# Optimization experiments

Hardware: AMD Instinct MI355X
Metric: run time of the kernel (lower is better)

## Reference

```python
import jax, jax.numpy as jnp
import numpy as np

N_NODES = 50000
N_EDGES = 800000
D_IN, D_HID, D_ENC = 256, 128, 64


def setup_inputs() -> dict:
    key = jax.random.key(0)
    ks = jax.random.split(key, 8)
    x = jax.random.normal(ks[0], (N_NODES, D_IN), dtype=jnp.float32)
    edge_index = jax.random.randint(ks[1], (2, N_EDGES), 0, N_NODES, dtype=jnp.int64)
    # GCNConv params: lin weight (no bias) + separate bias, stored as [in, out]
    W1 = jax.random.normal(ks[2], (D_IN, D_HID), dtype=jnp.float32) * (1.0 / np.sqrt(D_IN))
    b1 = jnp.zeros((D_HID,), dtype=jnp.float32)
    W2 = jax.random.normal(ks[3], (D_HID, D_ENC), dtype=jnp.float32) * (1.0 / np.sqrt(D_HID))
    b2 = jnp.zeros((D_ENC,), dtype=jnp.float32)
    Wfc = jax.random.normal(ks[4], (D_ENC, 1), dtype=jnp.float32) * (1.0 / np.sqrt(D_ENC))
    bfc = jnp.zeros((1,), dtype=jnp.float32)
    return {"x": x, "edge_index": edge_index, "W1": W1, "b1": b1,
            "W2": W2, "b2": b2, "Wfc": Wfc, "bfc": bfc}


def gcn_conv(x, W, b, row, col, norm, n_nodes):
    """PyG GCNConv (normalize=True): D^-1/2 (A+I) D^-1/2 X W + b."""
    h = x @ W                                   # [N, out]
    msg = h[row] * norm[:, None]                # [E+N, out] gather + scale
    out = jax.ops.segment_sum(msg, col, num_segments=n_nodes)  # scatter-add
    return out + b


def gcn_norm(edge_index, n_nodes, dtype):
    loop = jnp.arange(n_nodes, dtype=edge_index.dtype)
    row = jnp.concatenate([edge_index[0], loop])  # sources
    col = jnp.concatenate([edge_index[1], loop])  # targets
    deg = jax.ops.segment_sum(jnp.ones_like(col, dtype=dtype), col,
                              num_segments=n_nodes)
    dinv = jnp.where(deg > 0, jax.lax.rsqrt(jnp.maximum(deg, 1e-12)), 0.0)
    norm = dinv[row] * dinv[col]
    return row, col, norm


def reference(x, edge_index, W1, b1, W2, b2, Wfc, bfc):
    n = x.shape[0]
    row, col, norm = gcn_norm(edge_index, n, x.dtype)
    h = gcn_conv(x, W1, b1, row, col, norm, n)
    h = jax.nn.relu(h)
    # dropout p=0 / eval mode: identity
    h = gcn_conv(h, W2, b2, row, col, norm, n)
    out = jax.nn.sigmoid(h @ Wfc + bfc)          # [N, 1]
    return out
```

## Files before the change

### kernel.cpp

```cpp
#include <hip/hip_runtime.h>
#include <cmath>

#define N_NODES 50000
#define N_EDGES 800000
#define D_IN 256
#define D_HID 128
#define D_ENC 64
#define NBUK 128
#define BSH 9
#define BMSK 511
#define BCAP 16384
#define PB_EPT 8

typedef short short8 __attribute__((ext_vector_type(8)));
typedef float floatx4 __attribute__((ext_vector_type(4)));
typedef float floatx8 __attribute__((ext_vector_type(8)));
typedef unsigned short ushort8v __attribute__((ext_vector_type(8)));

static __device__ __forceinline__ unsigned short f2bf(float f) {
    unsigned int u = __float_as_uint(f);
    unsigned int r = (u + 0x7FFFu + ((u >> 16) & 1u)) >> 16;
    return (unsigned short)r;
}
static __device__ __forceinline__ float bf2f(unsigned short u) {
    return __uint_as_float(((unsigned int)u) << 16);
}
static __device__ __forceinline__ floatx8 bf2f8(ushort8v u) {
    floatx8 f;
#pragma unroll
    for (int j = 0; j < 8; ++j) f[j] = bf2f(u[j]);
    return f;
}

static __device__ __forceinline__ void wswz(const float* __restrict__ W,
                                            unsigned short* __restrict__ Wsw,
                                            int t, int K, int N) {
    int KS = K / 32;
    int lane = t & 63;
    int ks   = (t >> 6) % KS;
    int ct   = (t >> 6) / KS;
    int m = lane & 15, quad = lane >> 4;
    int kbase = ks * 32 + quad * 8;
    int col   = ct * 16 + m;
#pragma unroll
    for (int j = 0; j < 8; ++j)
        Wsw[t * 8 + j] = f2bf(W[(size_t)(kbase + j) * N + col]);
}

__global__ void part_k(const int* __restrict__ rows, const int* __restrict__ cols,
                       int* __restrict__ bcur, unsigned int* __restrict__ brecs,
                       const float* __restrict__ W1, const float* __restrict__ W2,
                       unsigned short* __restrict__ Wsw1, unsigned short* __restrict__ Wsw2) {
    __shared__ int h[NBUK], base[NBUK];
    int t = blockIdx.x * blockDim.x + threadIdx.x;
    if (t < 4096) wswz(W1, Wsw1, t, D_IN, D_HID);
    else if (t < 5120) wswz(W2, Wsw2, t - 4096, D_HID, D_ENC);

    int e0 = blockIdx.x * (256 * PB_EPT);
    if (threadIdx.x < NBUK) h[threadIdx.x] = 0;
    __syncthreads();
    int src[PB_EPT], dst[PB_EPT];
#pragma unroll
    for (int j = 0; j < PB_EPT; ++j) {
        int e = e0 + j * 256 + threadIdx.x;
        if (e < N_EDGES) {
            src[j] = rows[e]; dst[j] = cols[e];
            atomicAdd(&h[dst[j] >> BSH], 1);
        } else dst[j] = -1;
    }
    __syncthreads();
    if (threadIdx.x < NBUK) {
        int c = h[threadIdx.x];
        base[threadIdx.x] = threadIdx.x * BCAP + (c ? atomicAdd(&bcur[threadIdx.x], c) : 0);
        h[threadIdx.x] = 0;
    }
    __syncthreads();
#pragma unroll
    for (int j = 0; j < PB_EPT; ++j) {
        if (dst[j] >= 0) {
            int b = dst[j] >> BSH;
            int r = base[b] + atomicAdd(&h[b], 1);
            if (r < (b + 1) * BCAP)
                brecs[r] = ((unsigned int)src[j] << BSH) | (unsigned int)(dst[j] & BMSK);
        }
    }
}

__global__ __launch_bounds__(512) void bucket_csr_k(const unsigned int* __restrict__ brecs,
                                                    const int* __restrict__ bcur,
                                                    int* __restrict__ rowptr,
                                                    int* __restrict__ rowcnt,
                                                    int* __restrict__ srcs,
                                                    float* __restrict__ dinv) {
    __shared__ int s[512];
    __shared__ int cur[512];
    int b = blockIdx.x;
    int cb = bcur[b]; if (cb > BCAP) cb = BCAP;
    int ebeg = b * BCAP, eend = ebeg + cb;
    int tid = threadIdx.x;
    s[tid] = 0;
    __syncthreads();
    for (int e = ebeg + tid; e < eend; e += 512)
        atomicAdd(&s[brecs[e] & BMSK], 1);
    __syncthreads();
    int v = s[tid];
    for (int off = 1; off < 512; off <<= 1) {
        int t = (tid >= off) ? s[tid - off] : 0;
        __syncthreads();
        s[tid] += t;
        __syncthreads();
    }
    int excl = s[tid] - v;
    cur[tid] = excl;
    int node = (b << BSH) + tid;
    if (node < N_NODES) {
        rowptr[node] = ebeg + excl;
        rowcnt[node] = v;
        dinv[node] = rsqrtf((float)(v + 1));
    }
    __syncthreads();
    for (int e = ebeg + tid; e < eend; e += 512) {
        unsigned int rec = brecs[e];
        int p = atomicAdd(&cur[rec & BMSK], 1);
        srcs[ebeg + p] = (int)(rec >> BSH);
    }
}

template<int K, int N, bool IN_BF16>
__global__ __launch_bounds__(256) void gemm_mfma_k(const void* __restrict__ Xv,
                                                   const unsigned short* __restrict__ Wsw,
                                                   const float* __restrict__ dinv,
                                                   unsigned short* __restrict__ H, int n) {
    constexpr int KS = K / 32, CT = N / 16, KP = K + 8;
    __shared__ unsigned short As[64 * KP];
    int row0 = blockIdx.x * 64;
    if (IN_BF16) {
        const ushort8v* X8 = (const ushort8v*)Xv;
        constexpr int NF8 = 64 * (K / 8);
        for (int idx = threadIdx.x; idx < NF8; idx += 256) {
            int r = idx / (K / 8), c8 = idx % (K / 8);
            int gr = row0 + r;
            ushort8v v = (gr < n) ? X8[(size_t)gr * (K / 8) + c8] : (ushort8v)0;
            *(ushort8v*)&As[r * KP + c8 * 8] = v;
        }
    } else {
        const float4* X4 = (const float4*)Xv;
        constexpr int NF4 = 64 * (K / 4);
        for (int idx = threadIdx.x; idx < NF4; idx += 256) {
            int r = idx / (K / 4), c4 = idx % (K / 4);
            int gr = row0 + r;
            float4 v = (gr < n) ? X4[(size_t)gr * (K / 4) + c4] : float4{0, 0, 0, 0};
            ushort4 p;
            p.x = f2bf(v.x); p.y = f2bf(v.y); p.z = f2bf(v.z); p.w = f2bf(v.w);
            *(ushort4*)&As[r * KP + c4 * 4] = p;
        }
    }
    __syncthreads();

    int w    = threadIdx.x >> 6;
    int lane = threadIdx.x & 63;
    int m    = lane & 15;
    int quad = lane >> 4;

    floatx4 acc[CT];
#pragma unroll
    for (int ct = 0; ct < CT; ++ct)
#pragma unroll
        for (int i = 0; i < 4; ++i) acc[ct][i] = 0.0f;

#pragma unroll
    for (int ks = 0; ks < KS; ++ks) {
        short8 af = *(const short8*)&As[(w * 16 + m) * KP + ks * 32 + quad * 8];
#pragma unroll
        for (int ct = 0; ct < CT; ++ct) {
            short8 bf = *(const short8*)&Wsw[(size_t)((ct * KS + ks) * 64 + lane) * 8];
            acc[ct] = __builtin_amdgcn_mfma_f32_16x16x32_bf16(af, bf, acc[ct], 0, 0, 0);
        }
    }

    int rbase = row0 + w * 16 + quad * 4;
    float dv[4];
#pragma unroll
    for (int reg = 0; reg < 4; ++reg) {
        int r = rbase + reg;
        dv[reg] = (r < n) ? dinv[r] : 0.0f;
    }
#pragma unroll
    for (int ct = 0; ct < CT; ++ct)
#pragma unroll
        for (int reg = 0; reg < 4; ++reg) {
            int r = rbase + reg;
            if (r < n) H[(size_t)r * N + ct * 16 + m] = f2bf(acc[ct][reg] * dv[reg]);
        }
}

__global__ __launch_bounds__(256) void g1g2_k(const ushort8v* __restrict__ hs,
                                              const int* __restrict__ rowptr,
                                              const int* __restrict__ rowcnt,
                                              const int* __restrict__ srcs,
                                              const float* __restrict__ dinv,
                                              const float4* __restrict__ b1_4,
                                              const unsigned short* __restrict__ Wsw2,
                                              unsigned short* __restrict__ h2) {
    constexpr int KP = D_HID + 8;
    __shared__ unsigned short As[16 * KP];
    int nodeb = blockIdx.x * 16;
    int ln = threadIdx.x >> 4;
    int d8 = threadIdx.x & 15;
    int node = nodeb + ln;
    int beg = rowptr[node];
    int end = beg + rowcnt[node];
    floatx8 a0 = {0,0,0,0,0,0,0,0}, a1 = a0, a2 = a0, a3 = a0;
    int i = beg;
    for (; i + 4 <= end; i += 4) {
        int s0 = srcs[i], s1 = srcs[i + 1], s2 = srcs[i + 2], s3 = srcs[i + 3];
        a0 += bf2f8(hs[(size_t)s0 * 16 + d8]);
        a1 += bf2f8(hs[(size_t)s1 * 16 + d8]);
        a2 += bf2f8(hs[(size_t)s2 * 16 + d8]);
        a3 += bf2f8(hs[(size_t)s3 * 16 + d8]);
    }
    for (; i < end; ++i)
        a0 += bf2f8(hs[(size_t)srcs[i] * 16 + d8]);
    floatx8 acc = a0 + a1 + a2 + a3 + bf2f8(hs[(size_t)node * 16 + d8]);
    float di = dinv[node];
    float4 bA = b1_4[d8 * 2], bB = b1_4[d8 * 2 + 1];
    ushort8v r;
    r[0] = f2bf(fmaxf(di * acc[0] + bA.x, 0.0f));
    r[1] = f2bf(fmaxf(di * acc[1] + bA.y, 0.0f));
    r[2] = f2bf(fmaxf(di * acc[2] + bA.z, 0.0f));
    r[3] = f2bf(fmaxf(di * acc[3] + bA.w, 0.0f));
    r[4] = f2bf(fmaxf(di * acc[4] + bB.x, 0.0f));
    r[5] = f2bf(fmaxf(di * acc[5] + bB.y, 0.0f));
    r[6] = f2bf(fmaxf(di * acc[6] + bB.z, 0.0f));
    r[7] = f2bf(fmaxf(di * acc[7] + bB.w, 0.0f));
    *(ushort8v*)&As[ln * KP + d8 * 8] = r;
    __syncthreads();

    constexpr int KS = D_HID / 32;
    int w    = threadIdx.x >> 6;
    int lane = threadIdx.x & 63;
    int m = lane & 15, quad = lane >> 4;
    floatx4 acc2 = {0, 0, 0, 0};
#pragma unroll
    for (int ks = 0; ks < KS; ++ks) {
        short8 af = *(const short8*)&As[m * KP + ks * 32 + quad * 8];
        short8 bf = *(const short8*)&Wsw2[(size_t)((w * KS + ks) * 64 + lane) * 8];
        acc2 = __builtin_amdgcn_mfma_f32_16x16x32_bf16(af, bf, acc2, 0, 0, 0);
    }
#pragma unroll
    for (int reg = 0; reg < 4; ++reg) {
        int nn = nodeb + quad * 4 + reg;
        h2[(size_t)nn * D_ENC + w * 16 + m] = f2bf(acc2[reg] * dinv[nn]);
    }
}

__global__ void gather2_k(const ushort8v* __restrict__ hs, const int* __restrict__ rowptr,
                          const int* __restrict__ rowcnt, const int* __restrict__ srcs,
                          const float* __restrict__ dinv,
                          const float4* __restrict__ b4, const float4* __restrict__ Wfc4,
                          const float* __restrict__ bfc, float* __restrict__ out) {
    int node = blockIdx.x * 32 + (threadIdx.x >> 3);
    int d8   = threadIdx.x & 7;
    if (node >= N_NODES) return;
    int beg = rowptr[node];
    int end = beg + rowcnt[node];
    floatx8 a0 = {0,0,0,0,0,0,0,0}, a1 = a0, a2 = a0, a3 = a0;
    int i = beg;
    for (; i + 4 <= end; i += 4) {
        int s0 = srcs[i], s1 = srcs[i + 1], s2 = srcs[i + 2], s3 = srcs[i + 3];
        a0 += bf2f8(hs[(size_t)s0 * 8 + d8]);
        a1 += bf2f8(hs[(size_t)s1 * 8 + d8]);
        a2 += bf2f8(hs[(size_t)s2 * 8 + d8]);
        a3 += bf2f8(hs[(size_t)s3 * 8 + d8]);
    }
    for (; i < end; ++i)
        a0 += bf2f8(hs[(size_t)srcs[i] * 8 + d8]);
    floatx8 acc = a0 + a1 + a2 + a3 + bf2f8(hs[(size_t)node * 8 + d8]);
    float di = dinv[node];
    float4 bA = b4[d8 * 2], bB = b4[d8 * 2 + 1];
    float4 wA = Wfc4[d8 * 2], wB = Wfc4[d8 * 2 + 1];
    float p = (di * acc[0] + bA.x) * wA.x + (di * acc[1] + bA.y) * wA.y
            + (di * acc[2] + bA.z) * wA.z + (di * acc[3] + bA.w) * wA.w
            + (di * acc[4] + bB.x) * wB.x + (di * acc[5] + bB.y) * wB.y
            + (di * acc[6] + bB.z) * wB.z + (di * acc[7] + bB.w) * wB.w;
#pragma unroll
    for (int off = 4; off; off >>= 1) p += __shfl_down(p, off, 8);
    if (d8 == 0) out[node] = 1.0f / (1.0f + expf(-(p + bfc[0])));
}

extern "C" void kernel_launch(void* const* d_in, const int* in_sizes, int n_in,
                              void* d_out, int out_size, void* d_ws, size_t ws_size,
                              hipStream_t stream) {
    const float* x   = (const float*)d_in[0];
    const int*   ei  = (const int*)d_in[1];
    const float* W1  = (const float*)d_in[2];
    const float* b1  = (const float*)d_in[3];
    const float* W2  = (const float*)d_in[4];
    const float* b2  = (const float*)d_in[5];
    const float* Wfc = (const float*)d_in[6];
    const float* bfc = (const float*)d_in[7];
    float* out = (float*)d_out;

    const int* rows = ei;
    const int* cols = ei + N_EDGES;

    float* ws     = (float*)d_ws;
    float* dinv   = ws;
    int*   rowptr = (int*)(ws + 50048);
    int*   rowcnt = rowptr + 50048;
    int*   bcur   = rowcnt + 50048;
    int*   srcs   = bcur + 128;
    unsigned int* brecs = (unsigned int*)(srcs + NBUK * BCAP);
    unsigned short* h1 = (unsigned short*)(brecs + NBUK * BCAP);
    unsigned short* h2 = h1 + (size_t)N_NODES * D_HID;
    unsigned short* Wsw1 = h2 + (size_t)N_NODES * D_ENC;
    unsigned short* Wsw2 = Wsw1 + (size_t)D_IN * D_HID;

    hipMemsetAsync(bcur, 0, NBUK * sizeof(int), stream);
    part_k<<<(N_EDGES + 256 * PB_EPT - 1) / (256 * PB_EPT), 256, 0, stream>>>(
        rows, cols, bcur, brecs, W1, W2, Wsw1, Wsw2);
    bucket_csr_k<<<(N_NODES + 511) / 512, 512, 0, stream>>>(brecs, bcur, rowptr, rowcnt, srcs, dinv);

    gemm_mfma_k<D_IN, D_HID, false><<<(N_NODES + 63) / 64, 256, 0, stream>>>(x, Wsw1, dinv, h1, N_NODES);

    g1g2_k<<<N_NODES / 16, 256, 0, stream>>>((const ushort8v*)h1, rowptr, rowcnt, srcs, dinv,
                                             (const float4*)b1, Wsw2, h2);

    gather2_k<<<(N_NODES + 31) / 32, 256, 0, stream>>>((const ushort8v*)h2, rowptr, rowcnt, srcs, dinv,
                                                       (const float4*)b2, (const float4*)Wfc,
                                                       bfc, out);
}
```

Measured before the change: 198.2 us.

## Sort nodes by degree within buckets to balance gather work per block

The CSR build kernel now computes a per-bucket degree histogram (clamped at 63) and writes a node permutation sorted by in-degree. Both aggregation kernels process nodes in this permuted order so that nodes with similar neighbor counts share a wavefront, reducing divergence and idle lanes in the gather loops. Padding slots with -1 are skipped. The fp32-to-bf16 conversion in the GEMM load also switches to the packed HIP intrinsic. In exchange, adjacent threads no longer touch adjacent node rows, so output writes become scattered, and one thread per block runs a serial 64-entry scan.

```diff
diff --git a/kernel.cpp b/kernel.cpp
--- a/kernel.cpp
+++ b/kernel.cpp
@@ -1,4 +1,5 @@
 #include <hip/hip_runtime.h>
+#include <hip/hip_bf16.h>
 #include <cmath>
 
 #define N_NODES 50000
@@ -11,6 +12,8 @@
 #define BMSK 511
 #define BCAP 16384
 #define PB_EPT 8
+#define NVBUK 98
+#define PSLOTS (NVBUK * 512)
 
 typedef short short8 __attribute__((ext_vector_type(8)));
 typedef float floatx4 __attribute__((ext_vector_type(4)));
@@ -91,14 +94,17 @@
                                                     int* __restrict__ rowptr,
                                                     int* __restrict__ rowcnt,
                                                     int* __restrict__ srcs,
-                                                    float* __restrict__ dinv) {
+                                                    float* __restrict__ dinv,
+                                                    int* __restrict__ perm) {
     __shared__ int s[512];
     __shared__ int cur[512];
+    __shared__ int dh[64], db[64];
     int b = blockIdx.x;
     int cb = bcur[b]; if (cb > BCAP) cb = BCAP;
     int ebeg = b * BCAP, eend = ebeg + cb;
     int tid = threadIdx.x;
     s[tid] = 0;
+    if (tid < 64) dh[tid] = 0;
     __syncthreads();
     for (int e = ebeg + tid; e < eend; e += 512)
         atomicAdd(&s[brecs[e] & BMSK], 1);
@@ -113,12 +119,25 @@
     int excl = s[tid] - v;
     cur[tid] = excl;
     int node = (b << BSH) + tid;
-    if (node < N_NODES) {
+    bool valid = node < N_NODES;
+    int dcl = v > 63 ? 63 : v;
+    perm[(b << BSH) + tid] = -1;
+    if (valid) {
         rowptr[node] = ebeg + excl;
         rowcnt[node] = v;
         dinv[node] = rsqrtf((float)(v + 1));
-    }
-    __syncthreads();
+        atomicAdd(&dh[dcl], 1);
+    }
+    __syncthreads();
+    if (tid == 0) {
+        int a = 0;
+        for (int i = 0; i < 64; ++i) { int c = dh[i]; db[i] = a; a += c; dh[i] = 0; }
+    }
+    __syncthreads();
+    if (valid) {
+        int pos = db[dcl] + atomicAdd(&dh[dcl], 1);
+        perm[(b << BSH) + pos] = node;
+    }
     for (int e = ebeg + tid; e < eend; e += 512) {
         unsigned int rec = brecs[e];
         int p = atomicAdd(&cur[rec & BMSK], 1);
@@ -150,9 +169,10 @@
             int r = idx / (K / 4), c4 = idx % (K / 4);
             int gr = row0 + r;
             float4 v = (gr < n) ? X4[(size_t)gr * (K / 4) + c4] : float4{0, 0, 0, 0};
-            ushort4 p;
-            p.x = f2bf(v.x); p.y = f2bf(v.y); p.z = f2bf(v.z); p.w = f2bf(v.w);
-            *(ushort4*)&As[r * KP + c4 * 4] = p;
+            __hip_bfloat162 p0 = __float22bfloat162_rn(float2{v.x, v.y});
+            __hip_bfloat162 p1 = __float22bfloat162_rn(float2{v.z, v.w});
+            uint2 u; u.x = *(unsigned int*)&p0; u.y = *(unsigned int*)&p1;
+            *(uint2*)&As[r * KP + c4 * 4] = u;
         }
     }
     __syncthreads();
@@ -201,39 +221,46 @@
                                               const float* __restrict__ dinv,
                                               const float4* __restrict__ b1_4,
                                               const unsigned short* __restrict__ Wsw2,
+                                              const int* __restrict__ perm,
                                               unsigned short* __restrict__ h2) {
     constexpr int KP = D_HID + 8;
     __shared__ unsigned short As[16 * KP];
-    int nodeb = blockIdx.x * 16;
+    __shared__ int nid[16];
+    int slotb = blockIdx.x * 16;
     int ln = threadIdx.x >> 4;
     int d8 = threadIdx.x & 15;
-    int node = nodeb + ln;
-    int beg = rowptr[node];
-    int end = beg + rowcnt[node];
-    floatx8 a0 = {0,0,0,0,0,0,0,0}, a1 = a0, a2 = a0, a3 = a0;
-    int i = beg;
-    for (; i + 4 <= end; i += 4) {
-        int s0 = srcs[i], s1 = srcs[i + 1], s2 = srcs[i + 2], s3 = srcs[i + 3];
-        a0 += bf2f8(hs[(size_t)s0 * 16 + d8]);
-        a1 += bf2f8(hs[(size_t)s1 * 16 + d8]);
-        a2 += bf2f8(hs[(size_t)s2 * 16 + d8]);
-        a3 += bf2f8(hs[(size_t)s3 * 16 + d8]);
-    }
-    for (; i < end; ++i)
-        a0 += bf2f8(hs[(size_t)srcs[i] * 16 + d8]);
-    floatx8 acc = a0 + a1 + a2 + a3 + bf2f8(hs[(size_t)node * 16 + d8]);
-    float di = dinv[node];
-    float4 bA = b1_4[d8 * 2], bB = b1_4[d8 * 2 + 1];
-    ushort8v r;
-    r[0] = f2bf(fmaxf(di * acc[0] + bA.x, 0.0f));
-    r[1] = f2bf(fmaxf(di * acc[1] + bA.y, 0.0f));
-    r[2] = f2bf(fmaxf(di * acc[2] + bA.z, 0.0f));
-    r[3] = f2bf(fmaxf(di * acc[3] + bA.w, 0.0f));
-    r[4] = f2bf(fmaxf(di * acc[4] + bB.x, 0.0f));
-    r[5] = f2bf(fmaxf(di * acc[5] + bB.y, 0.0f));
-    r[6] = f2bf(fmaxf(di * acc[6] + bB.z, 0.0f));
-    r[7] = f2bf(fmaxf(di * acc[7] + bB.w, 0.0f));
-    *(ushort8v*)&As[ln * KP + d8 * 8] = r;
+    int node = perm[slotb + ln];
+    if (d8 == 0) nid[ln] = node;
+    if (node >= 0) {
+        int beg = rowptr[node];
+        int end = beg + rowcnt[node];
+        floatx8 a0 = {0,0,0,0,0,0,0,0}, a1 = a0, a2 = a0, a3 = a0;
+        int i = beg;
+        for (; i + 4 <= end; i += 4) {
+            int s0 = srcs[i], s1 = srcs[i + 1], s2 = srcs[i + 2], s3 = srcs[i + 3];
+            a0 += bf2f8(hs[(size_t)s0 * 16 + d8]);
+            a1 += bf2f8(hs[(size_t)s1 * 16 + d8]);
+            a2 += bf2f8(hs[(size_t)s2 * 16 + d8]);
+            a3 += bf2f8(hs[(size_t)s3 * 16 + d8]);
+        }
+        for (; i < end; ++i)
+            a0 += bf2f8(hs[(size_t)srcs[i] * 16 + d8]);
+        floatx8 acc = a0 + a1 + a2 + a3 + bf2f8(hs[(size_t)node * 16 + d8]);
+        float di = dinv[node];
+        float4 bA = b1_4[d8 * 2], bB = b1_4[d8 * 2 + 1];
+        ushort8v r;
+        r[0] = f2bf(fmaxf(di * acc[0] + bA.x, 0.0f));
+        r[1] = f2bf(fmaxf(di * acc[1] + bA.y, 0.0f));
+        r[2] = f2bf(fmaxf(di * acc[2] + bA.z, 0.0f));
+        r[3] = f2bf(fmaxf(di * acc[3] + bA.w, 0.0f));
+        r[4] = f2bf(fmaxf(di * acc[4] + bB.x, 0.0f));
+        r[5] = f2bf(fmaxf(di * acc[5] + bB.y, 0.0f));
+        r[6] = f2bf(fmaxf(di * acc[6] + bB.z, 0.0f));
+        r[7] = f2bf(fmaxf(di * acc[7] + bB.w, 0.0f));
+        *(ushort8v*)&As[ln * KP + d8 * 8] = r;
+    } else {
+        *(ushort8v*)&As[ln * KP + d8 * 8] = (ushort8v)0;
+    }
     __syncthreads();
 
     constexpr int KS = D_HID / 32;
@@ -249,19 +276,21 @@
     }
 #pragma unroll
     for (int reg = 0; reg < 4; ++reg) {
-        int nn = nodeb + quad * 4 + reg;
-        h2[(size_t)nn * D_ENC + w * 16 + m] = f2bf(acc2[reg] * dinv[nn]);
+        int nn = nid[quad * 4 + reg];
+        if (nn >= 0)
+            h2[(size_t)nn * D_ENC + w * 16 + m] = f2bf(acc2[reg] * dinv[nn]);
     }
 }
 
 __global__ void gather2_k(const ushort8v* __restrict__ hs, const int* __restrict__ rowptr,
                           const int* __restrict__ rowcnt, const int* __restrict__ srcs,
-                          const float* __restrict__ dinv,
+                          const float* __restrict__ dinv, const int* __restrict__ perm,
                           const float4* __restrict__ b4, const float4* __restrict__ Wfc4,
                           const float* __restrict__ bfc, float* __restrict__ out) {
-    int node = blockIdx.x * 32 + (threadIdx.x >> 3);
+    int slot = blockIdx.x * 32 + (threadIdx.x >> 3);
     int d8   = threadIdx.x & 7;
-    if (node >= N_NODES) return;
+    int node = perm[slot];
+    if (node < 0) return;
     int beg = rowptr[node];
     int end = beg + rowcnt[node];
     floatx8 a0 = {0,0,0,0,0,0,0,0}, a1 = a0, a2 = a0, a3 = a0;
@@ -308,7 +337,8 @@
     float* dinv   = ws;
     int*   rowptr = (int*)(ws + 50048);
     int*   rowcnt = rowptr + 50048;
-    int*   bcur   = rowcnt + 50048;
+    int*   perm   = rowcnt + 50048;
+    int*   bcur   = perm + PSLOTS;
     int*   srcs   = bcur + 128;
     unsigned int* brecs = (unsigned int*)(srcs + NBUK * BCAP);
     unsigned short* h1 = (unsigned short*)(brecs + NBUK * BCAP);
@@ -319,14 +349,14 @@
     hipMemsetAsync(bcur, 0, NBUK * sizeof(int), stream);
     part_k<<<(N_EDGES + 256 * PB_EPT - 1) / (256 * PB_EPT), 256, 0, stream>>>(
         rows, cols, bcur, brecs, W1, W2, Wsw1, Wsw2);
-    bucket_csr_k<<<(N_NODES + 511) / 512, 512, 0, stream>>>(brecs, bcur, rowptr, rowcnt, srcs, dinv);
+    bucket_csr_k<<<NVBUK, 512, 0, stream>>>(brecs, bcur, rowptr, rowcnt, srcs, dinv, perm);
 
     gemm_mfma_k<D_IN, D_HID, false><<<(N_NODES + 63) / 64, 256, 0, stream>>>(x, Wsw1, dinv, h1, N_NODES);
 
-    g1g2_k<<<N_NODES / 16, 256, 0, stream>>>((const ushort8v*)h1, rowptr, rowcnt, srcs, dinv,
-                                             (const float4*)b1, Wsw2, h2);
-
-    gather2_k<<<(N_NODES + 31) / 32, 256, 0, stream>>>((const ushort8v*)h2, rowptr, rowcnt, srcs, dinv,
-                                                       (const float4*)b2, (const float4*)Wfc,
-                                                       bfc, out);
-}
+    g1g2_k<<<PSLOTS / 16, 256, 0, stream>>>((const ushort8v*)h1, rowptr, rowcnt, srcs, dinv,
+                                            (const float4*)b1, Wsw2, perm, h2);
+
+    gather2_k<<<PSLOTS / 32, 256, 0, stream>>>((const ushort8v*)h2, rowptr, rowcnt, srcs, dinv, perm,
+                                               (const float4*)b2, (const float4*)Wfc,
+                                               bfc, out);
+}
```

Measured after the change: 206.0 us. 3.9% more time.
